# Optimization experiments

Hardware: AMD Instinct MI355X
Metric: run time of the kernel (lower is better)

## Reference

```python
import jax, jax.numpy as jnp
import numpy as np

N_NODES = 100000
N_EDGES = 1200000
D = 64          # hidden_feat_dim == out_feat_dim
D_CELL = 16     # cell_feat_dim
HID = 256       # MLP hidden width (from MLP(..., 256, ...))
N_TGT = 50000


def setup_inputs() -> dict:
    key = jax.random.key(0)
    ks = jax.random.split(key, 13)
    inv = lambda d: 1.0 / np.sqrt(d)
    return {
        "h": jax.random.normal(ks[0], (N_NODES, D), jnp.float32),
        "cell_feat": jax.random.normal(ks[1], (N_NODES, D_CELL), jnp.float32),
        "src": jax.random.randint(ks[2], (N_EDGES,), 0, N_NODES, jnp.int32),
        "dst": jax.random.randint(ks[3], (N_EDGES,), 0, N_NODES, jnp.int32),
        "targets": jax.random.randint(ks[4], (N_TGT,), 0, N_NODES, jnp.int32),
        "Wn1": jax.random.normal(ks[5], (D, HID), jnp.float32) * inv(D),
        "bn1": jnp.zeros((HID,), jnp.float32),
        "Wn2": jax.random.normal(ks[6], (HID, D), jnp.float32) * inv(HID),
        "bn2": jnp.zeros((D,), jnp.float32),
        "Ws1": jax.random.normal(ks[7], (D_CELL, HID), jnp.float32) * inv(D_CELL),
        "bs1": jnp.zeros((HID,), jnp.float32),
        "Ws2": jax.random.normal(ks[8], (HID, D), jnp.float32) * inv(HID),
        "bs2": jnp.zeros((D,), jnp.float32),
    }


def _mlp2(x, W1, b1, W2, b2):
    # MLP(d_in, 256, d_out) with LeakyReLU(negative_slope=0) == ReLU
    return jax.nn.relu(x @ W1 + b1) @ W2 + b2


def reference(h, cell_feat, src, dst, targets,
              Wn1, bn1, Wn2, bn2, Ws1, bs1, Ws2, bs2):
    # PathConv forward, even level_id > 0, flag_attn=False:
    #   pull(copy_src('h','m'), cell_msg_reduce, apply_cell_func) on 'cell' edges
    N = h.shape[0]
    m = h[src]  # gather edge messages [E, D]
    # cell_msg_reduce: per-dst, per-channel softmax over incoming messages
    mmax = jax.ops.segment_max(m, dst, num_segments=N)          # [N, D]
    mmax = jnp.where(jnp.isfinite(mmax), mmax, 0.0)             # isolated nodes
    e = jnp.exp(m - mmax[dst])                                  # [E, D]
    den = jax.ops.segment_sum(e, dst, num_segments=N)           # [N, D]
    num = jax.ops.segment_sum(e * m, dst, num_segments=N)       # sum(msg*softmax)
    h_neigh1 = num / jnp.where(den == 0.0, 1.0, den)            # [N, D]
    # apply_cell_func: fc_cell_self(cell_feat) + fc_cell_neigh(h_neigh1)
    h_new = _mlp2(cell_feat, Ws1, bs1, Ws2, bs2) + _mlp2(h_neigh1, Wn1, bn1, Wn2, bn2)
    h_new = jax.nn.relu(h_new)  # self.activation
    return h_new[targets]
```

## Files before the change

kernel.cpp:

```cpp
#include <hip/hip_runtime.h>

#define NN 100000
#define NE 1200000
#define DD 64
#define DC 16
#define DH 256
#define NT 50000
#define MAXDEG 64

typedef __attribute__((ext_vector_type(8))) short bf16x8;
typedef __attribute__((ext_vector_type(4))) short bf16x4;
typedef __attribute__((ext_vector_type(4))) float f32x4;

__device__ __forceinline__ unsigned short f2bf(float x) {
    unsigned int u = __float_as_uint(x);
    return (unsigned short)((u + 0x7FFFu + ((u >> 16) & 1u)) >> 16);
}
__device__ __forceinline__ float bf2f(unsigned short b) {
    return __uint_as_float(((unsigned int)b) << 16);
}

__device__ __forceinline__ void split8t(const float* p, bf16x8& hi, bf16x8& lo) {
    f32x4 a = *reinterpret_cast<const f32x4*>(p);
    f32x4 b = *reinterpret_cast<const f32x4*>(p + 4);
    #pragma unroll
    for (int j = 0; j < 4; ++j) {
        unsigned short h = (unsigned short)(__float_as_uint(a[j]) >> 16);
        hi[j] = (short)h;
        lo[j] = (short)(__float_as_uint(a[j] - bf2f(h)) >> 16);
    }
    #pragma unroll
    for (int j = 0; j < 4; ++j) {
        unsigned short h = (unsigned short)(__float_as_uint(b[j]) >> 16);
        hi[4 + j] = (short)h;
        lo[4 + j] = (short)(__float_as_uint(b[j] - bf2f(h)) >> 16);
    }
}

__device__ __forceinline__ bf16x8 zero8() {
    return bf16x8{0, 0, 0, 0, 0, 0, 0, 0};
}
__device__ __forceinline__ bf16x8 pad8(bf16x4 v) {
    return bf16x8{v[0], v[1], v[2], v[3], 0, 0, 0, 0};
}

#define N_W1NT 16384
#define N_W1ST 8192
#define N_W2N  16384
#define N_W2S  16384
#define N_PACK (N_W1NT + N_W1ST + N_W2N + N_W2S)
#define N_PREP NN

__global__ __launch_bounds__(256) void prep_k(
    const float* __restrict__ Wn1, const float* __restrict__ Ws1,
    const float* __restrict__ Wn2, const float* __restrict__ Ws2,
    unsigned short* __restrict__ W1nT, unsigned short* __restrict__ W1sT,
    unsigned short* __restrict__ W2n,  unsigned short* __restrict__ W2s,
    int* __restrict__ ifl, int* __restrict__ deg)
{
    int tid = blockIdx.x * 256 + threadIdx.x;
    if (tid < NN) ifl[tid] = -1;
    if (tid < NT + 16) deg[tid] = 0;
    if (tid >= N_PACK) return;
    float v; unsigned short* ph; int idx;
    if (tid < N_W1NT) {
        idx = tid;
        int j = idx & 7, l = (idx >> 3) & 63, rest = idx >> 9;
        int ks = rest & 1, c = rest >> 1;
        int feat = ks * 32 + ((l >> 4) << 3) + j, hid = (c << 4) + (l & 15);
        v = Wn1[(size_t)feat * DH + hid];
        ph = W1nT;
    } else if (tid < N_W1NT + N_W1ST) {
        idx = tid - N_W1NT;
        int j = idx & 7, l = (idx >> 3) & 63, c = idx >> 9;
        int k = ((l >> 4) << 3) + j, hid = (c << 4) + (l & 15);
        v = (k < DC) ? Ws1[(size_t)k * DH + hid] : 0.0f;
        ph = W1sT;
    } else if (tid < N_W1NT + N_W1ST + N_W2N) {
        idx = tid - N_W1NT - N_W1ST;
        int j = idx & 3, l = (idx >> 2) & 63, rest = idx >> 8;
        int u = rest & 3, c = rest >> 2;
        int row = (c << 4) + ((l >> 4) << 2) + j, col = (u << 4) + (l & 15);
        v = Wn2[(size_t)row * DD + col];
        ph = W2n;
    } else {
        idx = tid - N_W1NT - N_W1ST - N_W2N;
        int j = idx & 3, l = (idx >> 2) & 63, rest = idx >> 8;
        int u = rest & 3, c = rest >> 2;
        int row = (c << 4) + ((l >> 4) << 2) + j, col = (u << 4) + (l & 15);
        v = Ws2[(size_t)row * DD + col];
        ph = W2s;
    }
    ph[idx] = f2bf(v);
}

__global__ __launch_bounds__(256) void mark_wl_k(
    const int* __restrict__ tg, int* __restrict__ ifl, int* __restrict__ cnt)
{
    int i = blockIdx.x * 256 + threadIdx.x;
    int lane = threadIdx.x & 63;
    bool claim = false;
    int t = 0;
    if (i < NT) {
        t = tg[i];
        claim = (atomicCAS(&ifl[t], -1, -2) == -1);
    }
    unsigned long long mask = __ballot(claim);
    if (mask == 0ull) return;
    int nclaim = __popcll(mask);
    int leader = __ffsll((unsigned long long)mask) - 1;
    int base = 0;
    if (lane == leader) base = atomicAdd(cnt, nclaim);
    base = __shfl(base, leader);
    if (claim) {
        int rank = __popcll(mask & ((1ull << lane) - 1ull));
        ifl[t] = base + rank;
    }
}

#define NE4 (NE / 4)
#define N_SCAT (NE4 > NT ? NE4 : NT)

__global__ __launch_bounds__(256) void scatter_tgw_k(
    const int4* __restrict__ src4, const int4* __restrict__ dst4,
    const int* __restrict__ ifl, const int* __restrict__ tg,
    int* __restrict__ tgw, int* __restrict__ deg, int* __restrict__ csr)
{
    int tid = blockIdx.x * 256 + threadIdx.x;
    if (tid < NE4) {
        int4 d = dst4[tid];
        int4 s = src4[tid];
        int w;
        w = ifl[d.x]; if (w >= 0) { int sl = atomicAdd(&deg[w], 1); if (sl < MAXDEG) csr[w * MAXDEG + sl] = s.x; }
        w = ifl[d.y]; if (w >= 0) { int sl = atomicAdd(&deg[w], 1); if (sl < MAXDEG) csr[w * MAXDEG + sl] = s.y; }
        w = ifl[d.z]; if (w >= 0) { int sl = atomicAdd(&deg[w], 1); if (sl < MAXDEG) csr[w * MAXDEG + sl] = s.z; }
        w = ifl[d.w]; if (w >= 0) { int sl = atomicAdd(&deg[w], 1); if (sl < MAXDEG) csr[w * MAXDEG + sl] = s.w; }
    }
    if (tid < NT) tgw[tid] = ifl[tg[tid]];
}

__global__ __launch_bounds__(256) void reduce_k(
    const float* __restrict__ h, const int* __restrict__ csr,
    const int* __restrict__ deg, const int* __restrict__ cnt,
    float* __restrict__ hn_c)
{
    int gw = (blockIdx.x * 256 + threadIdx.x) >> 6;
    int lane = threadIdx.x & 63;
    if (gw >= cnt[0]) return;
    int g = min(deg[gw], MAXDEG);
    int sid = csr[gw * MAXDEG + lane];
    if (lane >= g) sid = 0;
    const int e4 = lane >> 4, c4 = lane & 15;

    f32x4 accd = {0.f, 0.f, 0.f, 0.f}, accn = {0.f, 0.f, 0.f, 0.f};
    for (int base = 0; base < g; base += 16) {
        f32x4 m[4];
        bool  val[4];
        #pragma unroll
        for (int bb = 0; bb < 4; ++bb) {
            int idx = base + bb * 4 + e4;
            val[bb] = (idx < g);
            if (base + bb * 4 < g) {
                int s = __shfl(sid, idx);
                m[bb] = *reinterpret_cast<const f32x4*>(
                            h + (size_t)s * DD + c4 * 4);
            } else {
                m[bb] = f32x4{0.f, 0.f, 0.f, 0.f};
                val[bb] = false;
            }
        }
        #pragma unroll
        for (int bb = 0; bb < 4; ++bb) {
            #pragma unroll
            for (int r = 0; r < 4; ++r) {
                float ex = __expf(m[bb][r]);
                ex = val[bb] ? ex : 0.f;
                accd[r] += ex;
                accn[r] = fmaf(ex, m[bb][r], accn[r]);
            }
        }
    }
    #pragma unroll
    for (int r = 0; r < 4; ++r) {
        accd[r] += __shfl_xor(accd[r], 16);
        accn[r] += __shfl_xor(accn[r], 16);
        accd[r] += __shfl_xor(accd[r], 32);
        accn[r] += __shfl_xor(accn[r], 32);
    }
    if (lane < 16) {
        f32x4 o;
        #pragma unroll
        for (int r = 0; r < 4; ++r)
            o[r] = (accd[r] == 0.f) ? 0.f : accn[r] / accd[r];
        *reinterpret_cast<f32x4*>(hn_c + (size_t)gw * DD + c4 * 4) = o;
    }
}

#define NT64 ((NT + 63) / 64)

__global__ __launch_bounds__(256, 4) void mfma_mlp_k(
    const float* __restrict__ hn_c, const int* __restrict__ tgw,
    const float* __restrict__ cellf, const int* __restrict__ tg,
    const unsigned short* __restrict__ W1nT, const unsigned short* __restrict__ W1sT,
    const unsigned short* __restrict__ W2n,  const unsigned short* __restrict__ W2s,
    const float* __restrict__ bn1, const float* __restrict__ bs1,
    const float* __restrict__ bn2, const float* __restrict__ bs2,
    float* __restrict__ out)
{
    __shared__ float X[64][84];

    const int tid = threadIdx.x;
    const int wv = tid >> 6, ln = tid & 63;
    const int l16 = ln & 15, kb = (ln >> 4) << 3;
    const int rbase = blockIdx.x * 64;

    {
        int r = tid >> 2, seg = tid & 3;
        int row = rbase + r; if (row >= NT) row = NT - 1;
        int w = tgw[row];
        const float* hp = hn_c + (size_t)w * DD + seg * 16;
        *reinterpret_cast<f32x4*>(&X[r][seg * 16])      = *reinterpret_cast<const f32x4*>(hp);
        *reinterpret_cast<f32x4*>(&X[r][seg * 16 + 4])  = *reinterpret_cast<const f32x4*>(hp + 4);
        *reinterpret_cast<f32x4*>(&X[r][seg * 16 + 8])  = *reinterpret_cast<const f32x4*>(hp + 8);
        *reinterpret_cast<f32x4*>(&X[r][seg * 16 + 12]) = *reinterpret_cast<const f32x4*>(hp + 12);
        int t2 = tg[row];
        *reinterpret_cast<f32x4*>(&X[r][64 + seg * 4]) =
            *reinterpret_cast<const f32x4*>(cellf + (size_t)t2 * DC + seg * 4);
    }
    __syncthreads();

    bf16x8 xh[2], xl[2], sxh, sxl;
    #pragma unroll
    for (int ks = 0; ks < 2; ++ks)
        split8t(&X[wv * 16 + l16][ks * 32 + kb], xh[ks], xl[ks]);
    sxh = zero8(); sxl = zero8();
    if (ln < 32)
        split8t(&X[wv * 16 + l16][64 + kb], sxh, sxl);

    f32x4 accY[4];
    #pragma unroll
    for (int u = 0; u < 4; ++u) accY[u] = f32x4{0.f, 0.f, 0.f, 0.f};

    #pragma unroll
    for (int cg = 0; cg < 16; ++cg) {
        f32x4 a1 = *reinterpret_cast<const f32x4*>(bn1 + cg * 16 + ((ln >> 4) << 2));
        #pragma unroll
        for (int ks = 0; ks < 2; ++ks) {
            bf16x8 wh = *reinterpret_cast<const bf16x8*>(W1nT + (((cg * 2 + ks) * 64 + ln) << 3));
            a1 = __builtin_amdgcn_mfma_f32_16x16x32_bf16(wh, xh[ks], a1, 0, 0, 0);
            a1 = __builtin_amdgcn_mfma_f32_16x16x32_bf16(wh, xl[ks], a1, 0, 0, 0);
        }
        f32x4 a1s = *reinterpret_cast<const f32x4*>(bs1 + cg * 16 + ((ln >> 4) << 2));
        {
            bf16x8 whs = *reinterpret_cast<const bf16x8*>(W1sT + ((cg * 64 + ln) << 3));
            a1s = __builtin_amdgcn_mfma_f32_16x16x32_bf16(whs, sxh, a1s, 0, 0, 0);
            a1s = __builtin_amdgcn_mfma_f32_16x16x32_bf16(whs, sxl, a1s, 0, 0, 0);
        }
        bf16x8 pah = zero8(), pal = zero8(), psh = zero8(), psl = zero8();
        #pragma unroll
        for (int r = 0; r < 4; ++r) {
            float d = fmaxf(a1[r], 0.f);
            unsigned short hh = (unsigned short)(__float_as_uint(d) >> 16);
            pah[r] = (short)hh;
            pal[r] = (short)(__float_as_uint(d - bf2f(hh)) >> 16);
            float ds = fmaxf(a1s[r], 0.f);
            unsigned short hs = (unsigned short)(__float_as_uint(ds) >> 16);
            psh[r] = (short)hs;
            psl[r] = (short)(__float_as_uint(ds - bf2f(hs)) >> 16);
        }
        #pragma unroll
        for (int u = 0; u < 4; ++u) {
            bf16x8 wpn = pad8(*reinterpret_cast<const bf16x4*>(W2n + (((cg * 4 + u) * 64 + ln) << 2)));
            accY[u] = __builtin_amdgcn_mfma_f32_16x16x32_bf16(pah, wpn, accY[u], 0, 0, 0);
            accY[u] = __builtin_amdgcn_mfma_f32_16x16x32_bf16(pal, wpn, accY[u], 0, 0, 0);
            bf16x8 wps = pad8(*reinterpret_cast<const bf16x4*>(W2s + (((cg * 4 + u) * 64 + ln) << 2)));
            accY[u] = __builtin_amdgcn_mfma_f32_16x16x32_bf16(psh, wps, accY[u], 0, 0, 0);
            accY[u] = __builtin_amdgcn_mfma_f32_16x16x32_bf16(psl, wps, accY[u], 0, 0, 0);
        }
    }

    {
        const int s4 = (ln >> 4) << 2;
        float b2[4];
        #pragma unroll
        for (int u = 0; u < 4; ++u)
            b2[u] = bn2[u * 16 + l16] + bs2[u * 16 + l16];
        #pragma unroll
        for (int u = 0; u < 4; ++u)
            #pragma unroll
            for (int r = 0; r < 4; ++r) {
                int rowg = rbase + wv * 16 + s4 + r;
                if (rowg < NT)
                    out[(size_t)rowg * DD + u * 16 + l16] =
                        fmaxf(accY[u][r] + b2[u], 0.f);
            }
    }
}

extern "C" void kernel_launch(void* const* d_in, const int* in_sizes, int n_in,
                              void* d_out, int out_size, void* d_ws, size_t ws_size,
                              hipStream_t stream)
{
    const float* h     = (const float*)d_in[0];
    const float* cellf = (const float*)d_in[1];
    const int*   src   = (const int*)d_in[2];
    const int*   dst   = (const int*)d_in[3];
    const int*   tg    = (const int*)d_in[4];
    const float* Wn1   = (const float*)d_in[5];
    const float* bn1   = (const float*)d_in[6];
    const float* Wn2   = (const float*)d_in[7];
    const float* bn2   = (const float*)d_in[8];
    const float* Ws1   = (const float*)d_in[9];
    const float* bs1   = (const float*)d_in[10];
    const float* Ws2   = (const float*)d_in[11];
    const float* bs2   = (const float*)d_in[12];
    float* out = (float*)d_out;

    int*   ifl  = (int*)d_ws;
    int*   deg  = ifl + NN;
    int*   cnt  = deg + NT;
    int*   tgw  = cnt + 16;
    int*   csr  = tgw + NT;
    float* hn_c = (float*)(csr + (size_t)NT * MAXDEG);
    size_t woff = ((size_t)((char*)(hn_c + (size_t)NT * DD) - (char*)d_ws) + 63)
                  & ~(size_t)63;
    unsigned short* W1nT = (unsigned short*)((char*)d_ws + woff);
    unsigned short* W1sT = W1nT + N_W1NT;
    unsigned short* W2n  = W1sT + N_W1ST;
    unsigned short* W2s  = W2n + N_W2N;

    prep_k<<<(N_PREP + 255) / 256, 256, 0, stream>>>(
        Wn1, Ws1, Wn2, Ws2, W1nT, W1sT, W2n, W2s, ifl, deg);

    mark_wl_k<<<(NT + 255) / 256, 256, 0, stream>>>(tg, ifl, cnt);

    scatter_tgw_k<<<(N_SCAT + 255) / 256, 256, 0, stream>>>(
        (const int4*)src, (const int4*)dst, ifl, tg, tgw, deg, csr);

    reduce_k<<<NT / 4, 256, 0, stream>>>(h, csr, deg, cnt, hn_c);

    mfma_mlp_k<<<NT64, 256, 0, stream>>>(hn_c, tgw, cellf, tg,
        W1nT, W1sT, W2n, W2s, bn1, bs1, bn2, bs2, out);
}
```

Before: 99.78 us.

## Pack MLP MFMA operands to remove zero padding and split hidden dim across waves

The MLP kernel stops feeding half-zero bf16 operands to the 16x16x32 MFMAs. The cell-feature layer folds the hi/lo split terms into one K=32 MFMA, and the two second-layer weight matrices are interleaved so a single MFMA covers both branches. Blocks now process 32 rows, with pairs of waves splitting the 256 hidden units and combining partial outputs through shared memory. This roughly halves MFMA count and weight loads per row, at the cost of an extra reduction barrier and LDS traffic.

```diff
diff --git a/kernel.cpp b/kernel.cpp
--- a/kernel.cpp
+++ b/kernel.cpp
@@ -9,7 +9,6 @@
 #define MAXDEG 64
 
 typedef __attribute__((ext_vector_type(8))) short bf16x8;
-typedef __attribute__((ext_vector_type(4))) short bf16x4;
 typedef __attribute__((ext_vector_type(4))) float f32x4;
 
 __device__ __forceinline__ unsigned short f2bf(float x) {
@@ -37,25 +36,17 @@
     }
 }
 
-__device__ __forceinline__ bf16x8 zero8() {
-    return bf16x8{0, 0, 0, 0, 0, 0, 0, 0};
-}
-__device__ __forceinline__ bf16x8 pad8(bf16x4 v) {
-    return bf16x8{v[0], v[1], v[2], v[3], 0, 0, 0, 0};
-}
-
 #define N_W1NT 16384
-#define N_W1ST 8192
-#define N_W2N  16384
-#define N_W2S  16384
-#define N_PACK (N_W1NT + N_W1ST + N_W2N + N_W2S)
+#define N_W1SP 8192
+#define N_W2C  32768
+#define N_PACK (N_W1NT + N_W1SP + N_W2C)
 #define N_PREP NN
 
 __global__ __launch_bounds__(256) void prep_k(
     const float* __restrict__ Wn1, const float* __restrict__ Ws1,
     const float* __restrict__ Wn2, const float* __restrict__ Ws2,
-    unsigned short* __restrict__ W1nT, unsigned short* __restrict__ W1sT,
-    unsigned short* __restrict__ W2n,  unsigned short* __restrict__ W2s,
+    unsigned short* __restrict__ W1nT, unsigned short* __restrict__ W1sP,
+    unsigned short* __restrict__ W2c,
     int* __restrict__ ifl, int* __restrict__ deg)
 {
     int tid = blockIdx.x * 256 + threadIdx.x;
@@ -70,26 +61,19 @@
         int feat = ks * 32 + ((l >> 4) << 3) + j, hid = (c << 4) + (l & 15);
         v = Wn1[(size_t)feat * DH + hid];
         ph = W1nT;
-    } else if (tid < N_W1NT + N_W1ST) {
+    } else if (tid < N_W1NT + N_W1SP) {
         idx = tid - N_W1NT;
         int j = idx & 7, l = (idx >> 3) & 63, c = idx >> 9;
         int k = ((l >> 4) << 3) + j, hid = (c << 4) + (l & 15);
-        v = (k < DC) ? Ws1[(size_t)k * DH + hid] : 0.0f;
-        ph = W1sT;
-    } else if (tid < N_W1NT + N_W1ST + N_W2N) {
-        idx = tid - N_W1NT - N_W1ST;
-        int j = idx & 3, l = (idx >> 2) & 63, rest = idx >> 8;
+        v = Ws1[(size_t)(k & 15) * DH + hid];
+        ph = W1sP;
+    } else {
+        idx = tid - N_W1NT - N_W1SP;
+        int j = idx & 7, l = (idx >> 3) & 63, rest = idx >> 9;
         int u = rest & 3, c = rest >> 2;
-        int row = (c << 4) + ((l >> 4) << 2) + j, col = (u << 4) + (l & 15);
-        v = Wn2[(size_t)row * DD + col];
-        ph = W2n;
-    } else {
-        idx = tid - N_W1NT - N_W1ST - N_W2N;
-        int j = idx & 3, l = (idx >> 2) & 63, rest = idx >> 8;
-        int u = rest & 3, c = rest >> 2;
-        int row = (c << 4) + ((l >> 4) << 2) + j, col = (u << 4) + (l & 15);
-        v = Ws2[(size_t)row * DD + col];
-        ph = W2s;
+        int row = (c << 4) + ((l >> 4) << 2) + (j & 3), col = (u << 4) + (l & 15);
+        v = (j < 4) ? Wn2[(size_t)row * DD + col] : Ws2[(size_t)row * DD + col];
+        ph = W2c;
     }
     ph[idx] = f2bf(v);
 }
@@ -196,53 +180,75 @@
     }
 }
 
-#define NT64 ((NT + 63) / 64)
-
-__global__ __launch_bounds__(256, 4) void mfma_mlp_k(
+#define NT32 ((NT + 31) / 32)
+
+__global__ __launch_bounds__(256, 6) void mfma_mlp_k(
     const float* __restrict__ hn_c, const int* __restrict__ tgw,
     const float* __restrict__ cellf, const int* __restrict__ tg,
-    const unsigned short* __restrict__ W1nT, const unsigned short* __restrict__ W1sT,
-    const unsigned short* __restrict__ W2n,  const unsigned short* __restrict__ W2s,
+    const unsigned short* __restrict__ W1nT, const unsigned short* __restrict__ W1sP,
+    const unsigned short* __restrict__ W2c,
     const float* __restrict__ bn1, const float* __restrict__ bs1,
     const float* __restrict__ bn2, const float* __restrict__ bs2,
     float* __restrict__ out)
 {
-    __shared__ float X[64][84];
+    __shared__ float shbuf[32 * 84];
+    float (*X)[84]      = reinterpret_cast<float(*)[84]>(shbuf);
+    float (*Ys)[16][68] = reinterpret_cast<float(*)[16][68]>(shbuf);
 
     const int tid = threadIdx.x;
     const int wv = tid >> 6, ln = tid & 63;
     const int l16 = ln & 15, kb = (ln >> 4) << 3;
-    const int rbase = blockIdx.x * 64;
+    const int sg = wv >> 1;
+    const int hf = wv & 1;
+    const int rbase = blockIdx.x * 32;
 
     {
-        int r = tid >> 2, seg = tid & 3;
+        int r = tid >> 3, seg = tid & 7;
         int row = rbase + r; if (row >= NT) row = NT - 1;
         int w = tgw[row];
-        const float* hp = hn_c + (size_t)w * DD + seg * 16;
-        *reinterpret_cast<f32x4*>(&X[r][seg * 16])      = *reinterpret_cast<const f32x4*>(hp);
-        *reinterpret_cast<f32x4*>(&X[r][seg * 16 + 4])  = *reinterpret_cast<const f32x4*>(hp + 4);
-        *reinterpret_cast<f32x4*>(&X[r][seg * 16 + 8])  = *reinterpret_cast<const f32x4*>(hp + 8);
-        *reinterpret_cast<f32x4*>(&X[r][seg * 16 + 12]) = *reinterpret_cast<const f32x4*>(hp + 12);
-        int t2 = tg[row];
-        *reinterpret_cast<f32x4*>(&X[r][64 + seg * 4]) =
-            *reinterpret_cast<const f32x4*>(cellf + (size_t)t2 * DC + seg * 4);
+        const float* hp = hn_c + (size_t)w * DD + seg * 8;
+        *reinterpret_cast<f32x4*>(&X[r][seg * 8])     = *reinterpret_cast<const f32x4*>(hp);
+        *reinterpret_cast<f32x4*>(&X[r][seg * 8 + 4]) = *reinterpret_cast<const f32x4*>(hp + 4);
+        if (seg < 4) {
+            int t2 = tg[row];
+            *reinterpret_cast<f32x4*>(&X[r][64 + seg * 4]) =
+                *reinterpret_cast<const f32x4*>(cellf + (size_t)t2 * DC + seg * 4);
+        }
     }
     __syncthreads();
 
-    bf16x8 xh[2], xl[2], sxh, sxl;
+    const float* xrow = X[sg * 16 + l16];
+    bf16x8 xh[2], xl[2];
     #pragma unroll
     for (int ks = 0; ks < 2; ++ks)
-        split8t(&X[wv * 16 + l16][ks * 32 + kb], xh[ks], xl[ks]);
-    sxh = zero8(); sxl = zero8();
-    if (ln < 32)
-        split8t(&X[wv * 16 + l16][64 + kb], sxh, sxl);
+        split8t(&xrow[ks * 32 + kb], xh[ks], xl[ks]);
+    bf16x8 sx;
+    {
+        const float* cp = &xrow[64 + (kb & 8)];
+        f32x4 a = *reinterpret_cast<const f32x4*>(cp);
+        f32x4 b = *reinterpret_cast<const f32x4*>(cp + 4);
+        #pragma unroll
+        for (int j = 0; j < 4; ++j) {
+            unsigned short hh = (unsigned short)(__float_as_uint(a[j]) >> 16);
+            sx[j] = (ln < 32) ? (short)hh
+                              : (short)(__float_as_uint(a[j] - bf2f(hh)) >> 16);
+        }
+        #pragma unroll
+        for (int j = 0; j < 4; ++j) {
+            unsigned short hh = (unsigned short)(__float_as_uint(b[j]) >> 16);
+            sx[4 + j] = (ln < 32) ? (short)hh
+                                  : (short)(__float_as_uint(b[j] - bf2f(hh)) >> 16);
+        }
+    }
+    __syncthreads();
 
     f32x4 accY[4];
     #pragma unroll
     for (int u = 0; u < 4; ++u) accY[u] = f32x4{0.f, 0.f, 0.f, 0.f};
 
     #pragma unroll
-    for (int cg = 0; cg < 16; ++cg) {
+    for (int c8 = 0; c8 < 8; ++c8) {
+        const int cg = hf * 8 + c8;
         f32x4 a1 = *reinterpret_cast<const f32x4*>(bn1 + cg * 16 + ((ln >> 4) << 2));
         #pragma unroll
         for (int ks = 0; ks < 2; ++ks) {
@@ -252,48 +258,50 @@
         }
         f32x4 a1s = *reinterpret_cast<const f32x4*>(bs1 + cg * 16 + ((ln >> 4) << 2));
         {
-            bf16x8 whs = *reinterpret_cast<const bf16x8*>(W1sT + ((cg * 64 + ln) << 3));
-            a1s = __builtin_amdgcn_mfma_f32_16x16x32_bf16(whs, sxh, a1s, 0, 0, 0);
-            a1s = __builtin_amdgcn_mfma_f32_16x16x32_bf16(whs, sxl, a1s, 0, 0, 0);
-        }
-        bf16x8 pah = zero8(), pal = zero8(), psh = zero8(), psl = zero8();
+            bf16x8 whs = *reinterpret_cast<const bf16x8*>(W1sP + ((cg * 64 + ln) << 3));
+            a1s = __builtin_amdgcn_mfma_f32_16x16x32_bf16(whs, sx, a1s, 0, 0, 0);
+        }
+        bf16x8 ph, pl;
         #pragma unroll
         for (int r = 0; r < 4; ++r) {
             float d = fmaxf(a1[r], 0.f);
             unsigned short hh = (unsigned short)(__float_as_uint(d) >> 16);
-            pah[r] = (short)hh;
-            pal[r] = (short)(__float_as_uint(d - bf2f(hh)) >> 16);
+            ph[r] = (short)hh;
+            pl[r] = (short)(__float_as_uint(d - bf2f(hh)) >> 16);
             float ds = fmaxf(a1s[r], 0.f);
             unsigned short hs = (unsigned short)(__float_as_uint(ds) >> 16);
-            psh[r] = (short)hs;
-            psl[r] = (short)(__float_as_uint(ds - bf2f(hs)) >> 16);
+            ph[4 + r] = (short)hs;
+            pl[4 + r] = (short)(__float_as_uint(ds - bf2f(hs)) >> 16);
         }
         #pragma unroll
         for (int u = 0; u < 4; ++u) {
-            bf16x8 wpn = pad8(*reinterpret_cast<const bf16x4*>(W2n + (((cg * 4 + u) * 64 + ln) << 2)));
-            accY[u] = __builtin_amdgcn_mfma_f32_16x16x32_bf16(pah, wpn, accY[u], 0, 0, 0);
-            accY[u] = __builtin_amdgcn_mfma_f32_16x16x32_bf16(pal, wpn, accY[u], 0, 0, 0);
-            bf16x8 wps = pad8(*reinterpret_cast<const bf16x4*>(W2s + (((cg * 4 + u) * 64 + ln) << 2)));
-            accY[u] = __builtin_amdgcn_mfma_f32_16x16x32_bf16(psh, wps, accY[u], 0, 0, 0);
-            accY[u] = __builtin_amdgcn_mfma_f32_16x16x32_bf16(psl, wps, accY[u], 0, 0, 0);
-        }
-    }
-
-    {
-        const int s4 = (ln >> 4) << 2;
-        float b2[4];
-        #pragma unroll
-        for (int u = 0; u < 4; ++u)
-            b2[u] = bn2[u * 16 + l16] + bs2[u * 16 + l16];
+            bf16x8 w2 = *reinterpret_cast<const bf16x8*>(W2c + (((cg * 4 + u) * 64 + ln) << 3));
+            accY[u] = __builtin_amdgcn_mfma_f32_16x16x32_bf16(ph, w2, accY[u], 0, 0, 0);
+            accY[u] = __builtin_amdgcn_mfma_f32_16x16x32_bf16(pl, w2, accY[u], 0, 0, 0);
+        }
+    }
+
+    if (hf == 1) {
         #pragma unroll
         for (int u = 0; u < 4; ++u)
             #pragma unroll
+            for (int r = 0; r < 4; ++r)
+                Ys[sg][(ln >> 4) * 4 + r][u * 16 + l16] = accY[u][r];
+    }
+    __syncthreads();
+    if (hf == 0) {
+        const int s4 = (ln >> 4) << 2;
+        #pragma unroll
+        for (int u = 0; u < 4; ++u) {
+            float b2 = bn2[u * 16 + l16] + bs2[u * 16 + l16];
+            #pragma unroll
             for (int r = 0; r < 4; ++r) {
-                int rowg = rbase + wv * 16 + s4 + r;
+                int rowg = rbase + sg * 16 + s4 + r;
                 if (rowg < NT)
                     out[(size_t)rowg * DD + u * 16 + l16] =
-                        fmaxf(accY[u][r] + b2[u], 0.f);
+                        fmaxf(accY[u][r] + Ys[sg][s4 + r][u * 16 + l16] + b2, 0.f);
             }
+        }
     }
 }
 
@@ -325,12 +333,11 @@
     size_t woff = ((size_t)((char*)(hn_c + (size_t)NT * DD) - (char*)d_ws) + 63)
                   & ~(size_t)63;
     unsigned short* W1nT = (unsigned short*)((char*)d_ws + woff);
-    unsigned short* W1sT = W1nT + N_W1NT;
-    unsigned short* W2n  = W1sT + N_W1ST;
-    unsigned short* W2s  = W2n + N_W2N;
+    unsigned short* W1sP = W1nT + N_W1NT;
+    unsigned short* W2c  = W1sP + N_W1SP;
 
     prep_k<<<(N_PREP + 255) / 256, 256, 0, stream>>>(
-        Wn1, Ws1, Wn2, Ws2, W1nT, W1sT, W2n, W2s, ifl, deg);
+        Wn1, Ws1, Wn2, Ws2, W1nT, W1sP, W2c, ifl, deg);
 
     mark_wl_k<<<(NT + 255) / 256, 256, 0, stream>>>(tg, ifl, cnt);
 
@@ -339,6 +346,6 @@
 
     reduce_k<<<NT / 4, 256, 0, stream>>>(h, csr, deg, cnt, hn_c);
 
-    mfma_mlp_k<<<NT64, 256, 0, stream>>>(hn_c, tgw, cellf, tg,
-        W1nT, W1sT, W2n, W2s, bn1, bs1, bn2, bs2, out);
-}
+    mfma_mlp_k<<<NT32, 256, 0, stream>>>(hn_c, tgw, cellf, tg,
+        W1nT, W1sP, W2c, bn1, bs1, bn2, bs2, out);
+}
```

Result: faster. 90.77 us (-9.0%).
